# Kernel tuning notes

Hardware: AMD Instinct MI355X
Metric: run time of the kernel (lower is better)

The kernel has to match this reference:

```python
import jax, jax.numpy as jnp
import numpy as np

B, N, D, R, W, H, I = 256, 2048, 128, 4, 1, 1024, 1024
CI = I + R * D                       # controller input size (1536)
IF = 2 * D * W + 2 * W + 1 + 4 * R + D * R   # interface size (787)
OPI = H + R * D                      # output_proj input (1536)


def _norm(v):
    # F.normalize(dim=-1): x / max(||x||, eps)
    return v / jnp.maximum(jnp.linalg.norm(v, axis=-1, keepdims=True), 1e-12)


def setup_inputs() -> dict:
    key = jax.random.key(0)
    ks = jax.random.split(key, 16)
    u = lambda k, shape, fan: jax.random.uniform(k, shape, jnp.float32, -1.0 / np.sqrt(fan), 1.0 / np.sqrt(fan))
    return {
        "x": jax.random.normal(ks[0], (B, I), jnp.float32),
        "memory": jax.random.normal(ks[1], (N, D), jnp.float32) * np.sqrt(2.0 / (N + D)),  # xavier-ish
        "usage": jax.random.uniform(ks[2], (N,), jnp.float32),          # usage in [0,1)
        "link": jax.random.normal(ks[3], (N, N), jnp.float32) * 0.01,   # non-trivial link state
        "W_ih": u(ks[4], (4 * H, CI), H),
        "W_hh": u(ks[5], (4 * H, H), H),
        "b_ih": u(ks[6], (4 * H,), H),
        "b_hh": u(ks[7], (4 * H,), H),
        "W_if": u(ks[8], (IF, H), H),
        "b_if": u(ks[9], (IF,), H),
        "W_out": u(ks[10], (H, OPI), OPI),
        "b_out": u(ks[11], (H,), OPI),
    }


def reference(x, memory, usage, link, W_ih, W_hh, b_ih, b_hh, W_if, b_if, W_out, b_out):
    # initial uniform read weights (prev state at first step)
    prev_rw = jnp.full((B, R, N), 1.0 / N, x.dtype)
    read_flat = (prev_rw @ memory).reshape(B, -1)                 # (B, R*D)
    cin = jnp.concatenate([x, read_flat], axis=-1)                # (B, CI)

    # single LSTM step, h0 = c0 = 0, torch gate order i,f,g,o
    g = cin @ W_ih.T + b_ih + b_hh
    gi, gf, gg, go = jnp.split(g, 4, axis=-1)
    c = jax.nn.sigmoid(gi) * jnp.tanh(gg)
    h = jax.nn.sigmoid(go) * jnp.tanh(c)                          # (B, H) controller out

    itf = h @ W_if.T + b_if                                       # (B, IF)
    o = 0
    write_vals = itf[:, o:o + D * W].reshape(B, W, D); o += D * W
    erase = jax.nn.sigmoid(itf[:, o:o + D * W]).reshape(B, W, D); o += D * W
    write_gates = jax.nn.sigmoid(itf[:, o:o + W]); o += W         # (B, W)
    alloc_gate = jax.nn.sigmoid(itf[:, o:o + 1]); o += 1          # (B, 1)
    o += W                                                        # free gates (parsed, unused)
    read_modes = jax.nn.softmax(itf[:, o:o + 3 * R].reshape(B, R, 3), -1); o += 3 * R
    read_str = jax.nn.softplus(itf[:, o:o + R]); o += R           # (B, R)
    read_keys = itf[:, o:o + D * R].reshape(B, R, D)

    # content addressing for the write (strength = 1)
    mem_n = _norm(memory)
    cw = jax.nn.softmax(_norm(write_vals.mean(1)) @ mem_n.T, -1)  # (B, N)

    # allocation weighting: sorted-usage cumprod (per source semantics)
    idx = jnp.argsort(usage)
    su = usage[idx]
    cp = jnp.cumprod(1.0 - su)
    alloc_s = jnp.concatenate([su[:1], su[1:] * cp[:-1]])
    alloc = jnp.zeros_like(usage).at[idx].set(alloc_s)[None, :] * alloc_gate  # (B, N)

    write_w = write_gates[:, :, None] * (0.5 * cw + 0.5 * alloc)[:, None, :]  # (B, W, N)

    # temporal link update: batch-mean of diag-masked outer product, decay 0.9
    lu = jnp.einsum('bwn,bwm->nm', write_w, write_w) / B
    lu = lu * (1.0 - jnp.eye(N, dtype=lu.dtype))
    link_new = link * 0.9 + lu * 0.1

    # memory write (erase then add, batch-mean)
    ev = erase * write_gates[:, :, None]
    av = write_vals * write_gates[:, :, None]
    erase_mat = jnp.einsum('bwn,bwd->nd', write_w, ev) / B
    add_mat = jnp.einsum('bwn,bwd->nd', write_w, av) / B
    mem_new = memory * (1.0 - erase_mat) + add_mat

    # read addressing on updated memory and updated link (all R heads vectorized)
    sim = jnp.einsum('brd,nd->brn', _norm(read_keys), _norm(mem_new))
    content_r = jax.nn.softmax(sim * read_str[:, :, None], -1)    # (B, R, N)
    backward_w = jnp.einsum('brn,nm->brm', prev_rw, link_new)     # mode 1: prev @ L
    forward_w = jnp.einsum('brn,mn->brm', prev_rw, link_new)      # mode 2: prev @ L^T
    new_rw = (read_modes[..., 0:1] * content_r
              + read_modes[..., 1:2] * backward_w
              + read_modes[..., 2:3] * forward_w)                 # (B, R, N)

    read_out = (new_rw @ mem_new).reshape(B, -1)                  # (B, R*D)
    out = jnp.concatenate([h, read_out], axis=-1) @ W_out.T + b_out
    return out
```

## Files before the change

kernel.cpp:

```cpp
#include <hip/hip_runtime.h>
#include <cmath>

#define DEVI __device__ __forceinline__

DEVI float sigm(float x){ return 1.f/(1.f+expf(-x)); }

typedef __attribute__((ext_vector_type(8))) _Float16 half8;
typedef __attribute__((ext_vector_type(4))) _Float16 half4;
typedef __attribute__((ext_vector_type(4))) float float4v;


__global__ void k_zero(float* __restrict__ p, int n){
  int i = blockIdx.x*256 + threadIdx.x;
  if (i < n) p[i] = 0.f;
}

__global__ __launch_bounds__(256) void k_stage1(
    const float* __restrict__ mem, float* __restrict__ cm, _Float16* __restrict__ mem_h)
{
  __shared__ float smem[4][132];
  const int blk = blockIdx.x, t = threadIdx.x;
  const int wv = t >> 6, lane = t & 63;
  int rbase = blk*16 + wv*4;
  float x0[4], x1[4], ss[4];
  #pragma unroll
  for (int u = 0; u < 4; u++){
    const float* a = mem + (size_t)(rbase+u)*128;
    x0[u] = a[lane]; x1[u] = a[lane+64];
  }
  #pragma unroll
  for (int u = 0; u < 4; u++) ss[u] = x0[u]*x0[u] + x1[u]*x1[u];
  #pragma unroll
  for (int o = 1; o < 64; o <<= 1){
    #pragma unroll
    for (int u = 0; u < 4; u++) ss[u] += __shfl_xor(ss[u], o);
  }
  float c0 = 0.f, c1 = 0.f;
  #pragma unroll
  for (int u = 0; u < 4; u++){
    float invn = 1.f / fmaxf(sqrtf(ss[u]), 1e-12f);
    mem_h[(size_t)(rbase+u)*128 + lane]      = (_Float16)(x0[u]*invn);
    mem_h[(size_t)(rbase+u)*128 + 64 + lane] = (_Float16)(x1[u]*invn);
    c0 += x0[u]; c1 += x1[u];
  }
  smem[wv][lane] = c0; smem[wv][64+lane] = c1;
  __syncthreads();
  if (t < 128) atomicAdd(&cm[t], smem[0][t]+smem[1][t]+smem[2][t]+smem[3][t]);
}

#define QA 264
#define QB 520
#define QB3 776

template<typename TB> struct BReg;
template<> struct BReg<_Float16>{
  half8 v;
  DEVI void load(const _Float16* p){ v = *(const half8*)p; }
  DEVI half8 get() const { return v; }
};
template<> struct BReg<float>{
  float4v a, b;
  DEVI void load(const float* p){ a = *(const float4v*)p; b = *(const float4v*)(p+4); }
  DEVI half8 get() const {
    half8 h;
    #pragma unroll
    for (int j = 0; j < 4; j++){ h[j] = (_Float16)a[j]; h[4+j] = (_Float16)b[j]; }
    return h;
  }
};

struct ARegX {
  float4v a, b; float sc;
  DEVI void load(const float* __restrict__ x, const float* __restrict__ cm, int row, int k){
    const float* p;
    if (k < 1024){ p = x + (size_t)row*1024 + k; sc = 1.f; }
    else         { p = cm + ((k - 1024) & 127); sc = (1.f/2048.f); }
    a = *(const float4v*)p; b = *(const float4v*)(p+4);
  }
  DEVI half8 get() const {
    half8 h;
    #pragma unroll
    for (int j = 0; j < 4; j++){ h[j] = (_Float16)(a[j]*sc); h[4+j] = (_Float16)(b[j]*sc); }
    return h;
  }
};

template<typename TB>
__global__ __launch_bounds__(256) void gemm_t(
    const _Float16* __restrict__ A, const TB* __restrict__ Bm, float* __restrict__ C,
    int M, int N, int K,
    const float* __restrict__ bias1, const float* __restrict__ bias2)
{
  __shared__ _Float16 Ah[2][8*QA];
  __shared__ _Float16 Bh[2][8*QB];
  const int tid = threadIdx.x;
  const int m0 = blockIdx.y*32, n0 = blockIdx.x*64;
  const int T = K >> 6;
  const int arow = tid >> 3, aq = tid & 7;
  const int brow = tid >> 3, bq = tid & 7;
  int nB0 = n0 + brow;      if (nB0 >= N) nB0 = N - 1;
  int nB1 = n0 + brow + 32; if (nB1 >= N) nB1 = N - 1;
  const _Float16* Aptr = A + (size_t)(m0 + arow)*K + aq*8;
  const TB* Bp0 = Bm + (size_t)nB0*K + bq*8;
  const TB* Bp1 = Bm + (size_t)nB1*K + bq*8;
  const int wA  = aq*QA + arow*8;
  const int wB0 = bq*QB + brow*8;
  const int wB1 = bq*QB + (brow+32)*8;
  const int wv_ = tid >> 6, lane = tid & 63;
  const int fq = lane >> 4, fr = lane & 15;
  const int m16 = (wv_ & 1)*16, nb = (wv_ >> 1)*32;

  half8 ra;
  BReg<TB> rb0, rb1;
  ra = *(const half8*)(Aptr);
  rb0.load(Bp0);
  rb1.load(Bp1);
  *(half8*)&Ah[0][wA]  = ra;
  *(half8*)&Bh[0][wB0] = rb0.get();
  *(half8*)&Bh[0][wB1] = rb1.get();
  __syncthreads();

  float4v acc0 = {0.f,0.f,0.f,0.f}, acc1 = {0.f,0.f,0.f,0.f};
  for (int t = 0; t < T; t++){
    const int cur = t & 1, nxt = cur ^ 1;
    if (t+1 < T){
      ra = *(const half8*)(Aptr + (t+1)*64);
      rb0.load(Bp0 + (t+1)*64);
      rb1.load(Bp1 + (t+1)*64);
    }
    #pragma unroll
    for (int s = 0; s < 2; s++){
      int q = s*4 + fq;
      half8 a  = *(half8*)&Ah[cur][q*QA + (m16+fr)*8];
      half8 b0 = *(half8*)&Bh[cur][q*QB + (nb+fr)*8];
      half8 b1 = *(half8*)&Bh[cur][q*QB + (nb+16+fr)*8];
      acc0 = __builtin_amdgcn_mfma_f32_16x16x32_f16(a, b0, acc0, 0, 0, 0);
      acc1 = __builtin_amdgcn_mfma_f32_16x16x32_f16(a, b1, acc1, 0, 0, 0);
    }
    if (t+1 < T){
      *(half8*)&Ah[nxt][wA]  = ra;
      *(half8*)&Bh[nxt][wB0] = rb0.get();
      *(half8*)&Bh[nxt][wB1] = rb1.get();
    }
    __syncthreads();
  }

  const int colA = n0 + nb + fr, colB = colA + 16;
  #pragma unroll
  for (int i = 0; i < 4; i++){
    int m = m0 + m16 + fq*4 + i;
    if (colA < N){
      float v = acc0[i];
      if (bias1) v += bias1[colA];
      if (bias2) v += bias2[colA];
      C[(size_t)m*N + colA] = v;
    }
    if (colB < N){
      float v = acc1[i];
      if (bias1) v += bias1[colB];
      if (bias2) v += bias2[colB];
      C[(size_t)m*N + colB] = v;
    }
  }
}

__global__ __launch_bounds__(256) void gemm_hro(
    const _Float16* __restrict__ Ah_, const _Float16* __restrict__ Aro,
    const float* __restrict__ Bm, float* __restrict__ C,
    const float* __restrict__ bias1)
{
  __shared__ _Float16 Ah[2][8*QA];
  __shared__ _Float16 Bh[2][8*QB];
  const int tid = threadIdx.x;
  const int m0 = blockIdx.y*32, n0 = blockIdx.x*64;
  const int T = 24;
  const int arow = tid >> 3, aq = tid & 7;
  const int brow = tid >> 3, bq = tid & 7;
  const int arw = m0 + arow;
  const float* Bp0 = Bm + (size_t)(n0 + brow)*1536 + bq*8;
  const float* Bp1 = Bm + (size_t)(n0 + brow + 32)*1536 + bq*8;
  const int wA  = aq*QA + arow*8;
  const int wB0 = bq*QB + brow*8;
  const int wB1 = bq*QB + (brow+32)*8;
  const int wv_ = tid >> 6, lane = tid & 63;
  const int fq = lane >> 4, fr = lane & 15;
  const int m16 = (wv_ & 1)*16, nb = (wv_ >> 1)*32;

  auto ldA = [&](int k) -> half8 {
    const _Float16* p = (k < 1024) ? (Ah_ + (size_t)arw*1024 + k)
                                   : (Aro + (size_t)arw*512 + (k - 1024));
    return *(const half8*)p;
  };

  half8 ra;
  BReg<float> rb0, rb1;
  ra = ldA(aq*8);
  rb0.load(Bp0);
  rb1.load(Bp1);
  *(half8*)&Ah[0][wA]  = ra;
  *(half8*)&Bh[0][wB0] = rb0.get();
  *(half8*)&Bh[0][wB1] = rb1.get();
  __syncthreads();

  float4v acc0 = {0.f,0.f,0.f,0.f}, acc1 = {0.f,0.f,0.f,0.f};
  for (int t = 0; t < T; t++){
    const int cur = t & 1, nxt = cur ^ 1;
    if (t+1 < T){
      ra = ldA(aq*8 + (t+1)*64);
      rb0.load(Bp0 + (t+1)*64);
      rb1.load(Bp1 + (t+1)*64);
    }
    #pragma unroll
    for (int s = 0; s < 2; s++){
      int q = s*4 + fq;
      half8 a  = *(half8*)&Ah[cur][q*QA + (m16+fr)*8];
      half8 b0 = *(half8*)&Bh[cur][q*QB + (nb+fr)*8];
      half8 b1 = *(half8*)&Bh[cur][q*QB + (nb+16+fr)*8];
      acc0 = __builtin_amdgcn_mfma_f32_16x16x32_f16(a, b0, acc0, 0, 0, 0);
      acc1 = __builtin_amdgcn_mfma_f32_16x16x32_f16(a, b1, acc1, 0, 0, 0);
    }
    if (t+1 < T){
      *(half8*)&Ah[nxt][wA]  = ra;
      *(half8*)&Bh[nxt][wB0] = rb0.get();
      *(half8*)&Bh[nxt][wB1] = rb1.get();
    }
    __syncthreads();
  }

  const int colA = n0 + nb + fr, colB = colA + 16;
  #pragma unroll
  for (int i = 0; i < 4; i++){
    int m = m0 + m16 + fq*4 + i;
    C[(size_t)m*1024 + colA] = acc0[i] + bias1[colA];
    C[(size_t)m*1024 + colB] = acc1[i] + bias1[colB];
  }
}

__global__ __launch_bounds__(256) void k_gemm_wwExp(
    const _Float16* __restrict__ A, const _Float16* __restrict__ Bm,
    float* __restrict__ C, float* __restrict__ rsum)
{
  __shared__ _Float16 Ah[2][8*QA];
  __shared__ _Float16 Bh[2][8*QB];
  const int tid = threadIdx.x;
  const int m0 = blockIdx.y*32, n0 = blockIdx.x*64;
  const int arow = tid >> 3, aq = tid & 7;
  const int brow = tid >> 3, bq = tid & 7;
  const _Float16* Aptr = A + (size_t)(m0 + arow)*128 + aq*8;
  const _Float16* Bp0 = Bm + (size_t)(n0 + brow)*128 + bq*8;
  const _Float16* Bp1 = Bm + (size_t)(n0 + brow + 32)*128 + bq*8;
  const int wA  = aq*QA + arow*8;
  const int wB0 = bq*QB + brow*8;
  const int wB1 = bq*QB + (brow+32)*8;
  const int wv_ = tid >> 6, lane = tid & 63;
  const int fq = lane >> 4, fr = lane & 15;
  const int m16 = (wv_ & 1)*16, nb = (wv_ >> 1)*32;

  half8 ra  = *(const half8*)(Aptr);
  half8 rb0 = *(const half8*)(Bp0);
  half8 rb1 = *(const half8*)(Bp1);
  *(half8*)&Ah[0][wA]  = ra;
  *(half8*)&Bh[0][wB0] = rb0;
  *(half8*)&Bh[0][wB1] = rb1;
  __syncthreads();

  float4v acc0 = {0.f,0.f,0.f,0.f}, acc1 = {0.f,0.f,0.f,0.f};
  for (int t = 0; t < 2; t++){
    const int cur = t & 1, nxt = cur ^ 1;
    if (t == 0){
      ra  = *(const half8*)(Aptr + 64);
      rb0 = *(const half8*)(Bp0 + 64);
      rb1 = *(const half8*)(Bp1 + 64);
    }
    #pragma unroll
    for (int s = 0; s < 2; s++){
      int q = s*4 + fq;
      half8 a  = *(half8*)&Ah[cur][q*QA + (m16+fr)*8];
      half8 b0 = *(half8*)&Bh[cur][q*QB + (nb+fr)*8];
      half8 b1 = *(half8*)&Bh[cur][q*QB + (nb+16+fr)*8];
      acc0 = __builtin_amdgcn_mfma_f32_16x16x32_f16(a, b0, acc0, 0, 0, 0);
      acc1 = __builtin_amdgcn_mfma_f32_16x16x32_f16(a, b1, acc1, 0, 0, 0);
    }
    if (t == 0){
      *(half8*)&Ah[nxt][wA]  = ra;
      *(half8*)&Bh[nxt][wB0] = rb0;
      *(half8*)&Bh[nxt][wB1] = rb1;
    }
    __syncthreads();
  }

  const int colA = n0 + nb + fr, colB = colA + 16;
  #pragma unroll
  for (int i = 0; i < 4; i++){
    int m = m0 + m16 + fq*4 + i;
    float e0 = expf(acc0[i]);
    float e1 = expf(acc1[i]);
    C[(size_t)m*2048 + colA] = e0;
    C[(size_t)m*2048 + colB] = e1;
    float rs = e0 + e1;
    #pragma unroll
    for (int o = 1; o < 16; o <<= 1) rs += __shfl_xor(rs, o);
    if (fr == 0) atomicAdd(&rsum[m], rs);
  }
}

__global__ __launch_bounds__(256) void k_big2(
    const float* __restrict__ x, const float* __restrict__ cm,
    const float* __restrict__ W,
    const float* __restrict__ b_ih, const float* __restrict__ b_hh,
    _Float16* __restrict__ h,
    const float* __restrict__ usage, float* __restrict__ alloc,
    const float* __restrict__ link, float* __restrict__ rsl, float* __restrict__ cslp)
{
  extern __shared__ char smraw[];
  const int blk = blockIdx.x, tid = threadIdx.x;
  const int wv = tid >> 6, lane = tid & 63;

  if (blk < 256){
    _Float16* AhP = (_Float16*)smraw;
    _Float16* BhP = (_Float16*)(smraw + 2*8*QA*sizeof(_Float16));
    const int SA = 8*QA, SB = 8*QB3;
    const int m0 = (blk >> 5)*32, c0 = (blk & 31)*32;
    const int T = 24;
    const int arow = tid >> 3, aq = tid & 7;
    const int brow = tid >> 3, bq = tid & 7;
    const int arw = m0 + arow;
    const float* Bpi = W + (size_t)(       c0 + brow)*1536 + bq*8;
    const float* Bpg = W + (size_t)(2048 + c0 + brow)*1536 + bq*8;
    const float* Bpo = W + (size_t)(3072 + c0 + brow)*1536 + bq*8;
    const int wA  = aq*QA + arow*8;
    const int wBi = bq*QB3 + brow*8;
    const int wBg = bq*QB3 + (32+brow)*8;
    const int wBo = bq*QB3 + (64+brow)*8;
    const int fq = lane >> 4, fr = lane & 15;
    const int m16 = (wv & 1)*16, c16 = (wv >> 1)*16;

    ARegX ax0, ax1;
    BReg<float> ri0, rg0, ro0, ri1, rg1, ro1;
    ax0.load(x, cm, arw, aq*8);
    ri0.load(Bpi); rg0.load(Bpg); ro0.load(Bpo);
    ax1.load(x, cm, arw, aq*8 + 64);
    ri1.load(Bpi + 64); rg1.load(Bpg + 64); ro1.load(Bpo + 64);
    *(half8*)&AhP[wA]  = ax0.get();
    *(half8*)&BhP[wBi] = ri0.get();
    *(half8*)&BhP[wBg] = rg0.get();
    *(half8*)&BhP[wBo] = ro0.get();
    __syncthreads();

    float4v acci = {0.f,0.f,0.f,0.f}, accg = {0.f,0.f,0.f,0.f}, acco = {0.f,0.f,0.f,0.f};
    for (int t = 0; t < T; t++){
      const int cur = t & 1, nxt = cur ^ 1;
      if (t+2 < T){
        if (cur == 0){
          ax0.load(x, cm, arw, aq*8 + (t+2)*64);
          ri0.load(Bpi + (t+2)*64); rg0.load(Bpg + (t+2)*64); ro0.load(Bpo + (t+2)*64);
        } else {
          ax1.load(x, cm, arw, aq*8 + (t+2)*64);
          ri1.load(Bpi + (t+2)*64); rg1.load(Bpg + (t+2)*64); ro1.load(Bpo + (t+2)*64);
        }
      }
      #pragma unroll
      for (int s = 0; s < 2; s++){
        int q = s*4 + fq;
        half8 a  = *(half8*)&AhP[cur*SA + q*QA + (m16+fr)*8];
        half8 bi = *(half8*)&BhP[cur*SB + q*QB3 + (c16+fr)*8];
        half8 bg = *(half8*)&BhP[cur*SB + q*QB3 + (32+c16+fr)*8];
        half8 bo = *(half8*)&BhP[cur*SB + q*QB3 + (64+c16+fr)*8];
        acci = __builtin_amdgcn_mfma_f32_16x16x32_f16(a, bi, acci, 0, 0, 0);
        accg = __builtin_amdgcn_mfma_f32_16x16x32_f16(a, bg, accg, 0, 0, 0);
        acco = __builtin_amdgcn_mfma_f32_16x16x32_f16(a, bo, acco, 0, 0, 0);
      }
      if (t+1 < T){
        if (nxt == 1){
          *(half8*)&AhP[SA + wA]  = ax1.get();
          *(half8*)&BhP[SB + wBi] = ri1.get();
          *(half8*)&BhP[SB + wBg] = rg1.get();
          *(half8*)&BhP[SB + wBo] = ro1.get();
        } else {
          *(half8*)&AhP[wA]  = ax0.get();
          *(half8*)&BhP[wBi] = ri0.get();
          *(half8*)&BhP[wBg] = rg0.get();
          *(half8*)&BhP[wBo] = ro0.get();
        }
      }
      __syncthreads();
    }

    const int col = c0 + c16 + fr;
    const float bi1 = b_ih[col]        + b_hh[col];
    const float bg1 = b_ih[2048 + col] + b_hh[2048 + col];
    const float bo1 = b_ih[3072 + col] + b_hh[3072 + col];
    #pragma unroll
    for (int i = 0; i < 4; i++){
      int m = m0 + m16 + fq*4 + i;
      float gi = acci[i] + bi1;
      float gg = accg[i] + bg1;
      float go = acco[i] + bo1;
      float c = sigm(gi) * tanhf(gg);
      h[(size_t)m*1024 + col] = (_Float16)(sigm(go) * tanhf(c));
    }
  } else if (blk < 512){
    float (*smem)[132] = (float(*)[132])smraw;
    int pb = blk - 256;
    int r0 = pb*8;
    int c0 = tid*8;
    float4v v0[8], v1[8];
    #pragma unroll
    for (int u = 0; u < 8; u++){
      const float* lp = link + (size_t)(r0+u)*2048 + c0;
      v0[u] = *(const float4v*)lp;
      v1[u] = *(const float4v*)(lp+4);
    }
    float colacc[8];
    #pragma unroll
    for (int j = 0; j < 8; j++) colacc[j] = 0.f;
    float rowpart[8];
    #pragma unroll
    for (int u = 0; u < 8; u++){
      float s = 0.f;
      #pragma unroll
      for (int j = 0; j < 4; j++){
        colacc[j]   += v0[u][j]; colacc[4+j] += v1[u][j];
        s += v0[u][j] + v1[u][j];
      }
      rowpart[u] = s;
    }
    #pragma unroll
    for (int o = 1; o < 64; o <<= 1){
      #pragma unroll
      for (int u = 0; u < 8; u++) rowpart[u] += __shfl_xor(rowpart[u], o);
    }
    if (lane == 0){
      #pragma unroll
      for (int u = 0; u < 8; u++) smem[wv][u] = rowpart[u];
    }
    __syncthreads();
    if (tid < 8) rsl[r0+tid] = smem[0][tid]+smem[1][tid]+smem[2][tid]+smem[3][tid];
    float4v w0, w1;
    #pragma unroll
    for (int j = 0; j < 4; j++){ w0[j] = colacc[j]; w1[j] = colacc[4+j]; }
    *(float4v*)&cslp[(size_t)pb*2048 + c0]     = w0;
    *(float4v*)&cslp[(size_t)pb*2048 + c0 + 4] = w1;
  } else {
    int n = (blk - 512)*4 + wv;
    float un = usage[n];
    float prod = 1.f;
    #pragma unroll
    for (int i = 0; i < 32; i++){
      int m = lane + i*64;
      float um = usage[m];
      bool before = (um < un) || (um == un && m < n);
      prod *= before ? (1.f - um) : 1.f;
    }
    #pragma unroll
    for (int o = 32; o > 0; o >>= 1) prod *= __shfl_xor(prod, o);
    if (lane == 0) alloc[n] = un * prod;
  }
}

DEVI float blockReduce128(float v, float* lds2){
  #pragma unroll
  for (int o = 32; o > 0; o >>= 1) v += __shfl_xor(v, o);
  int w = threadIdx.x >> 6;
  __syncthreads();
  if ((threadIdx.x & 63) == 0) lds2[w] = v;
  __syncthreads();
  return lds2[0] + lds2[1];
}

__global__ __launch_bounds__(128) void k_parse(const float* __restrict__ itf,
    _Float16* __restrict__ wv_h, float* __restrict__ ev, float* __restrict__ av,
    float* __restrict__ wg_, float* __restrict__ ag_,
    float* __restrict__ rm0, float* __restrict__ rm1, float* __restrict__ rm2,
    _Float16* __restrict__ rks_h)
{
  __shared__ float red[2];
  int b = blockIdx.x, t = threadIdx.x;
  const float* it = itf + (size_t)b*787;
  float wg = sigm(it[256]);
  float ag = sigm(it[257]);
  if (t == 0){ wg_[b] = wg; ag_[b] = ag; }
  float w = it[t];
  av[b*128 + t] = w * wg;
  ev[b*128 + t] = sigm(it[128 + t]) * wg;
  float ss = blockReduce128(w*w, red);
  float invwv = 1.f / fmaxf(sqrtf(ss), 1e-12f);
  wv_h[b*128 + t] = (_Float16)(w * invwv);
  if (t < 4){
    int rr = t;
    float m0v = it[259 + rr*3 + 0], m1v = it[259 + rr*3 + 1], m2v = it[259 + rr*3 + 2];
    float mx = fmaxf(m0v, fmaxf(m1v, m2v));
    float e0 = expf(m0v - mx), e1 = expf(m1v - mx), e2 = expf(m2v - mx);
    float inv = 1.f / (e0 + e1 + e2);
    rm0[b*4 + rr] = e0*inv; rm1[b*4 + rr] = e1*inv; rm2[b*4 + rr] = e2*inv;
  }
  #pragma unroll
  for (int rr = 0; rr < 4; rr++){
    float kv = it[275 + rr*128 + t];
    float ks = blockReduce128(kv*kv, red);
    float sx = it[271 + rr];
    float str = fmaxf(sx, 0.f) + log1pf(expf(-fabsf(sx)));
    float invk = 1.f / fmaxf(sqrtf(ks), 1e-12f);
    rks_h[((size_t)b*4 + rr)*128 + t] = (_Float16)(kv * invk * str);
  }
}

__global__ __launch_bounds__(256) void k_memupdate_fused(const float* __restrict__ ww,
    const float* __restrict__ ev, const float* __restrict__ av,
    const float* __restrict__ mem,
    const float* __restrict__ wg, const float* __restrict__ ag,
    const float* __restrict__ alloc, const float* __restrict__ rsum,
    const float* __restrict__ rsl, const float* __restrict__ cslp,
    _Float16* __restrict__ memn_h, _Float16* __restrict__ memnT_h,
    float* __restrict__ bwm, float* __restrict__ fwm)
{
  __shared__ float Ws[16][34];
  __shared__ float Es[16][132], Vs[16][132];
  __shared__ float lb[128], lf[128];
  __shared__ _Float16 Traw[32][132];
  __shared__ float tbs[256], c1s[256], c2s[256];
  __shared__ float allocL[32];
  __shared__ float sq[8][32], sd[8][32];
  __shared__ float cpart[8][32];
  __shared__ float bwL[32], fwL[32];
  __shared__ float sred[4];
  const int n0 = blockIdx.x*32;
  const int tid = threadIdx.x, tx = tid & 31, ty = tid >> 5;

  {
    float sa = 0.f;
    #pragma unroll
    for (int i = 0; i < 8; i++) sa += alloc[tid + i*256];
    #pragma unroll
    for (int o = 32; o > 0; o >>= 1) sa += __shfl_xor(sa, o);
    if ((tid & 63) == 0) sred[tid >> 6] = sa;
    if (tid < 128){ lb[tid] = 0.f; lf[tid] = 0.f; }
    if (tid < 32) allocL[tid] = alloc[n0 + tid];
    __syncthreads();
    sa = (sred[0]+sred[1]) + (sred[2]+sred[3]);
    float w = wg[tid], a = ag[tid];
    tbs[tid] = w*(0.5f + 0.5f*a*sa);
    c1s[tid] = 0.5f*w / rsum[tid];
    c2s[tid] = 0.5f*w*a;
  }
  {
    int col = n0 + tx;
    float s = 0.f;
    for (int p = ty*32; p < ty*32 + 32; p += 4){
      s += cslp[(size_t)(p+0)*2048 + col] + cslp[(size_t)(p+1)*2048 + col]
         + cslp[(size_t)(p+2)*2048 + col] + cslp[(size_t)(p+3)*2048 + col];
    }
    cpart[ty][tx] = s;
  }
  __syncthreads();

  const int wk = tid >> 4, wn = (tid & 15)*2;
  const int ek = tid >> 4, ec = (tid & 15)*8;
  float ae[4][4] = {}, aa[4][4] = {};
  float qp = 0.f, ddp = 0.f;
  for (int k0 = 0; k0 < 256; k0 += 16){
    float2 vw  = *(const float2*)(ww + (size_t)(k0+wk)*2048 + n0 + wn);
    float4 ve0 = *(const float4*)(ev + (size_t)(k0+ek)*128 + ec);
    float4 ve1 = *(const float4*)(ev + (size_t)(k0+ek)*128 + ec + 4);
    float4 va0 = *(const float4*)(av + (size_t)(k0+ek)*128 + ec);
    float4 va1 = *(const float4*)(av + (size_t)(k0+ek)*128 + ec + 4);
    __syncthreads();
    {
      float cb1 = c1s[k0+wk], cb2 = c2s[k0+wk];
      Ws[wk][wn]   = cb1*vw.x + cb2*allocL[wn];
      Ws[wk][wn+1] = cb1*vw.y + cb2*allocL[wn+1];
    }
    *(float4*)&Es[ek][ec] = ve0; *(float4*)&Es[ek][ec+4] = ve1;
    *(float4*)&Vs[ek][ec] = va0; *(float4*)&Vs[ek][ec+4] = va1;
    __syncthreads();
    #pragma unroll
    for (int k = 0; k < 16; k++){
      float a[4], e[4], v[4];
      #pragma unroll
      for (int i = 0; i < 4; i++) a[i] = Ws[k][ty*4+i];
      #pragma unroll
      for (int j = 0; j < 4; j++){ e[j] = Es[k][tx*4+j]; v[j] = Vs[k][tx*4+j]; }
      #pragma unroll
      for (int i = 0; i < 4; i++)
        #pragma unroll
        for (int j = 0; j < 4; j++){
          ae[i][j] = fmaf(a[i], e[j], ae[i][j]);
          aa[i][j] = fmaf(a[i], v[j], aa[i][j]);
        }
    }
    {
      float w0 = Ws[ty*2+0][tx], w1 = Ws[ty*2+1][tx];
      qp  = fmaf(tbs[k0+ty*2+0], w0, qp);  ddp = fmaf(w0, w0, ddp);
      qp  = fmaf(tbs[k0+ty*2+1], w1, qp);  ddp = fmaf(w1, w1, ddp);
    }
  }
  sq[ty][tx] = qp; sd[ty][tx] = ddp;
  __syncthreads();
  if (tid < 32){
    float q = 0.f, dd = 0.f, cs = 0.f;
    #pragma unroll
    for (int z = 0; z < 8; z++){ q += sq[z][tid]; dd += sd[z][tid]; cs += cpart[z][tid]; }
    float lus = (q - dd) * (1.f/256.f);
    bwL[tid] = (0.9f*cs + 0.1f*lus) * (1.f/2048.f);
    fwL[tid] = (0.9f*rsl[n0+tid] + 0.1f*lus) * (1.f/2048.f);
  }
  __syncthreads();

  float ab[4] = {0,0,0,0}, af[4] = {0,0,0,0};
  #pragma unroll
  for (int i = 0; i < 4; i++){
    int n = n0 + ty*4 + i;
    float bwn = bwL[ty*4+i], fwn = fwL[ty*4+i];
    float v[4]; float ss = 0.f;
    #pragma unroll
    for (int j = 0; j < 4; j++){
      int d = tx*4 + j;
      float em = ae[i][j]*(1.f/256.f), am = aa[i][j]*(1.f/256.f);
      float mv = mem[(size_t)n*128 + d]*(1.f - em) + am;
      v[j] = mv; ss += mv*mv;
      ab[j] = fmaf(bwn, mv, ab[j]);
      af[j] = fmaf(fwn, mv, af[j]);
    }
    #pragma unroll
    for (int o = 1; o < 32; o <<= 1) ss += __shfl_xor(ss, o);
    float invn = 1.f / fmaxf(sqrtf(ss), 1e-12f);
    half4 hn, hr;
    #pragma unroll
    for (int j = 0; j < 4; j++){ hn[j] = (_Float16)(v[j]*invn); hr[j] = (_Float16)v[j]; }
    *(half4*)(memn_h + (size_t)n*128 + tx*4) = hn;
    *(half4*)&Traw[ty*4+i][tx*4] = hr;
  }
  __syncthreads();
  {
    int d = tid >> 1, seg = (tid & 1)*16;
    half8 o0, o1;
    #pragma unroll
    for (int j = 0; j < 8; j++){ o0[j] = Traw[seg+j][d]; o1[j] = Traw[seg+8+j][d]; }
    *(half8*)(memnT_h + (size_t)d*2048 + n0 + seg)     = o0;
    *(half8*)(memnT_h + (size_t)d*2048 + n0 + seg + 8) = o1;
  }
  #pragma unroll
  for (int j = 0; j < 4; j++){
    atomicAdd(&lb[tx*4+j], ab[j]);
    atomicAdd(&lf[tx*4+j], af[j]);
  }
  __syncthreads();
  if (tid < 128){
    atomicAdd(&bwm[tid], lb[tid]);
    atomicAdd(&fwm[tid], lf[tid]);
  }
}

__global__ __launch_bounds__(256) void k_flash(
    const _Float16* __restrict__ Q, const _Float16* __restrict__ Kh,
    const _Float16* __restrict__ Vt,
    float* __restrict__ pacc, float* __restrict__ pm, float* __restrict__ pl)
{
  __shared__ _Float16 Pl[4][16][32];
  __shared__ float cmb[4][2080];
  __shared__ float scl[4][16];
  const int tid = threadIdx.x;
  const int qt = blockIdx.x >> 2, kc = blockIdx.x & 3;
  const int wv = tid >> 6, lane = tid & 63;
  const int fq = lane >> 4, fr = lane & 15;
  const int kw0 = kc*512 + wv*128;

  half8 aq[4];
  #pragma unroll
  for (int c = 0; c < 4; c++)
    aq[c] = *(const half8*)(Q + (size_t)(qt*16 + fr)*128 + c*32 + fq*8);

  float m[4] = {-3.0e38f,-3.0e38f,-3.0e38f,-3.0e38f};
  float l[4] = {0.f,0.f,0.f,0.f};
  float4v acc[8] = {};
  for (int s = 0; s < 4; s++){
    const int kb = kw0 + s*32;
    float4v S0 = {0,0,0,0}, S1 = {0,0,0,0};
    #pragma unroll
    for (int c = 0; c < 4; c++){
      half8 b0 = *(const half8*)(Kh + (size_t)(kb + fr)*128      + c*32 + fq*8);
      half8 b1 = *(const half8*)(Kh + (size_t)(kb + 16 + fr)*128 + c*32 + fq*8);
      S0 = __builtin_amdgcn_mfma_f32_16x16x32_f16(aq[c], b0, S0, 0, 0, 0);
      S1 = __builtin_amdgcn_mfma_f32_16x16x32_f16(aq[c], b1, S1, 0, 0, 0);
    }
    float mt[4], ps[4];
    #pragma unroll
    for (int i = 0; i < 4; i++) mt[i] = fmaxf(S0[i], S1[i]);
    #pragma unroll
    for (int o = 1; o < 16; o <<= 1){
      #pragma unroll
      for (int i = 0; i < 4; i++) mt[i] = fmaxf(mt[i], __shfl_xor(mt[i], o));
    }
    #pragma unroll
    for (int i = 0; i < 4; i++){
      float mn = fmaxf(m[i], mt[i]);
      float al = expf(m[i] - mn);
      float p0 = expf(S0[i] - mn), p1 = expf(S1[i] - mn);
      S0[i] = p0; S1[i] = p1;
      ps[i] = p0 + p1;
      l[i] *= al;
      m[i] = mn;
      #pragma unroll
      for (int c = 0; c < 8; c++) acc[c][i] *= al;
    }
    #pragma unroll
    for (int o = 1; o < 16; o <<= 1){
      #pragma unroll
      for (int i = 0; i < 4; i++) ps[i] += __shfl_xor(ps[i], o);
    }
    #pragma unroll
    for (int i = 0; i < 4; i++) l[i] += ps[i];
    #pragma unroll
    for (int i = 0; i < 4; i++){
      Pl[wv][fq*4+i][fr]      = (_Float16)S0[i];
      Pl[wv][fq*4+i][16 + fr] = (_Float16)S1[i];
    }
    half8 pf = *(half8*)&Pl[wv][fr][fq*8];
    #pragma unroll
    for (int c = 0; c < 8; c++){
      half8 bv = *(const half8*)(Vt + (size_t)(c*16 + fr)*2048 + kb + fq*8);
      acc[c] = __builtin_amdgcn_mfma_f32_16x16x32_f16(pf, bv, acc[c], 0, 0, 0);
    }
  }
  if (fr == 0){
    #pragma unroll
    for (int i = 0; i < 4; i++){
      cmb[wv][fq*4+i]      = m[i];
      cmb[wv][16 + fq*4+i] = l[i];
    }
  }
  #pragma unroll
  for (int c = 0; c < 8; c++)
    #pragma unroll
    for (int i = 0; i < 4; i++)
      cmb[wv][32 + (fq*4+i)*128 + c*16 + fr] = acc[c][i];
  __syncthreads();
  if (tid < 16){
    float mm = fmaxf(fmaxf(cmb[0][tid], cmb[1][tid]), fmaxf(cmb[2][tid], cmb[3][tid]));
    float ll = 0.f;
    #pragma unroll
    for (int w = 0; w < 4; w++){
      float e = expf(cmb[w][tid] - mm);
      scl[w][tid] = e;
      ll += e * cmb[w][16 + tid];
    }
    pm[blockIdx.x*16 + tid] = mm;
    pl[blockIdx.x*16 + tid] = ll;
  }
  __syncthreads();
  for (int e = tid; e < 2048; e += 256){
    int q = e >> 7;
    float a = scl[0][q]*cmb[0][32+e] + scl[1][q]*cmb[1][32+e]
            + scl[2][q]*cmb[2][32+e] + scl[3][q]*cmb[3][32+e];
    pacc[(size_t)blockIdx.x*2048 + e] = a;
  }
}

__global__ void k_ro(const float* __restrict__ pacc, const float* __restrict__ pm,
                     const float* __restrict__ pl,
                     const float* __restrict__ rm0, const float* __restrict__ rm1,
                     const float* __restrict__ rm2, const float* __restrict__ bwm,
                     const float* __restrict__ fwm, _Float16* __restrict__ ro){
  int idx = blockIdx.x*256 + threadIdx.x;
  int row = idx >> 7, d = idx & 127;
  int qt = row >> 4, q = row & 15;
  float mm = -3.0e38f;
  #pragma unroll
  for (int kc = 0; kc < 4; kc++) mm = fmaxf(mm, pm[(qt*4+kc)*16 + q]);
  float num = 0.f, den = 0.f;
  #pragma unroll
  for (int kc = 0; kc < 4; kc++){
    float e = expf(pm[(qt*4+kc)*16 + q] - mm);
    den += e * pl[(qt*4+kc)*16 + q];
    num += e * pacc[(size_t)(qt*4+kc)*2048 + q*128 + d];
  }
  float pv = num / den;
  ro[idx] = (_Float16)(rm0[row]*pv + rm1[row]*bwm[d] + rm2[row]*fwm[d]);
}


extern "C" void kernel_launch(void* const* d_in, const int* in_sizes, int n_in,
                              void* d_out, int out_size, void* d_ws, size_t ws_size,
                              hipStream_t stream)
{
  const float* x     = (const float*)d_in[0];
  const float* mem   = (const float*)d_in[1];
  const float* usage = (const float*)d_in[2];
  const float* link  = (const float*)d_in[3];
  const float* W_ih  = (const float*)d_in[4];
  const float* b_ih  = (const float*)d_in[6];
  const float* b_hh  = (const float*)d_in[7];
  const float* W_if  = (const float*)d_in[8];
  const float* b_if  = (const float*)d_in[9];
  const float* W_out = (const float*)d_in[10];
  const float* b_out = (const float*)d_in[11];
  float* out = (float*)d_out;
  float* ws  = (float*)d_ws;

  float* cm     = ws + 0;
  float* bwm    = ws + 2176;
  float* fwm    = ws + 2304;
  float* rsum   = ws + 2432;
  float* wg     = ws + 6784;
  float* ag     = ws + 7040;
  float* rm0    = ws + 7296;
  float* rm1    = ws + 8320;
  float* rm2    = ws + 9344;
  float* alloc  = ws + 10368;
  float* rsl    = ws + 12416;
  float* ev     = ws + 14464;
  float* av     = ws + 47232;
  float* itf    = ws + 1128576;
  float* ww     = ws + 1330048;
  float* pacc   = ws + 1854336;
  float* pm     = ws + 2378624;
  float* pl     = ws + 2382720;
  _Float16* wv_h    = (_Float16*)(ws + 2386816);
  _Float16* mem_h   = (_Float16*)(ws + 2403200);
  _Float16* memn_h  = (_Float16*)(ws + 2534272);
  _Float16* memnT_h = (_Float16*)(ws + 2665344);
  _Float16* rks_h   = (_Float16*)(ws + 2796416);
  _Float16* ro_h    = (_Float16*)(ws + 2861952);
  _Float16* h_h     = (_Float16*)(ws + 3255168);
  float* cslp       = ws + 3386240;

  const int SH_BIG2 = (2*8*QA + 2*8*QB3) * (int)sizeof(_Float16);

  k_zero<<<11, 256, 0, stream>>>(ws, 2688);

  k_stage1<<<128, 256, 0, stream>>>(mem, cm, mem_h);

  k_big2<<<1024, 256, SH_BIG2, stream>>>(x, cm, W_ih, b_ih, b_hh, h_h,
                                         usage, alloc, link, rsl, cslp);

  gemm_t<float><<<dim3(13,8), 256, 0, stream>>>(h_h, W_if, itf, 256, 787, 1024, b_if, nullptr);
  k_parse<<<256, 128, 0, stream>>>(itf, wv_h, ev, av, wg, ag, rm0, rm1, rm2, rks_h);

  k_gemm_wwExp<<<dim3(32,8), 256, 0, stream>>>(wv_h, mem_h, ww, rsum);

  k_memupdate_fused<<<64, 256, 0, stream>>>(ww, ev, av, mem, wg, ag, alloc, rsum,
                                            rsl, cslp, memn_h, memnT_h, bwm, fwm);

  k_flash<<<256, 256, 0, stream>>>(rks_h, memn_h, memnT_h, pacc, pm, pl);

  k_ro<<<512, 256, 0, stream>>>(pacc, pm, pl, rm0, rm1, rm2, bwm, fwm, ro_h);
  gemm_hro<<<dim3(16,8), 256, 0, stream>>>(h_h, ro_h, W_out, out, b_out);

  (void)in_sizes; (void)n_in; (void)out_size; (void)ws_size;
}
```

Baseline: 230.2 us.

## Deepen GEMM global prefetch to two stages and split flash over 8 key chunks

The two MFMA GEMM kernels now keep two sets of prefetch registers, so global loads are issued two k-tiles ahead instead of one, which hides more memory latency. The flash read kernel splits the 2048 memory rows into 8 chunks per query tile instead of 4, doubling its block count to fill more CUs. The reduction in k_ro and the workspace offsets are updated to match. In exchange the GEMMs use more registers and there is more partial-result traffic to combine.

```diff
diff --git a/kernel.cpp b/kernel.cpp
--- a/kernel.cpp
+++ b/kernel.cpp
@@ -110,23 +110,30 @@
   const int fq = lane >> 4, fr = lane & 15;
   const int m16 = (wv_ & 1)*16, nb = (wv_ >> 1)*32;
 
-  half8 ra;
-  BReg<TB> rb0, rb1;
-  ra = *(const half8*)(Aptr);
-  rb0.load(Bp0);
-  rb1.load(Bp1);
-  *(half8*)&Ah[0][wA]  = ra;
-  *(half8*)&Bh[0][wB0] = rb0.get();
-  *(half8*)&Bh[0][wB1] = rb1.get();
+  half8 ra0, ra1;
+  BReg<TB> rb00, rb10, rb01, rb11;
+  ra0 = *(const half8*)(Aptr);
+  rb00.load(Bp0); rb10.load(Bp1);
+  if (T > 1){
+    ra1 = *(const half8*)(Aptr + 64);
+    rb01.load(Bp0 + 64); rb11.load(Bp1 + 64);
+  }
+  *(half8*)&Ah[0][wA]  = ra0;
+  *(half8*)&Bh[0][wB0] = rb00.get();
+  *(half8*)&Bh[0][wB1] = rb10.get();
   __syncthreads();
 
   float4v acc0 = {0.f,0.f,0.f,0.f}, acc1 = {0.f,0.f,0.f,0.f};
   for (int t = 0; t < T; t++){
     const int cur = t & 1, nxt = cur ^ 1;
-    if (t+1 < T){
-      ra = *(const half8*)(Aptr + (t+1)*64);
-      rb0.load(Bp0 + (t+1)*64);
-      rb1.load(Bp1 + (t+1)*64);
+    if (t+2 < T){
+      if (cur == 0){
+        ra0 = *(const half8*)(Aptr + (t+2)*64);
+        rb00.load(Bp0 + (t+2)*64); rb10.load(Bp1 + (t+2)*64);
+      } else {
+        ra1 = *(const half8*)(Aptr + (t+2)*64);
+        rb01.load(Bp0 + (t+2)*64); rb11.load(Bp1 + (t+2)*64);
+      }
     }
     #pragma unroll
     for (int s = 0; s < 2; s++){
@@ -138,9 +145,15 @@
       acc1 = __builtin_amdgcn_mfma_f32_16x16x32_f16(a, b1, acc1, 0, 0, 0);
     }
     if (t+1 < T){
-      *(half8*)&Ah[nxt][wA]  = ra;
-      *(half8*)&Bh[nxt][wB0] = rb0.get();
-      *(half8*)&Bh[nxt][wB1] = rb1.get();
+      if (nxt == 1){
+        *(half8*)&Ah[1][wA]  = ra1;
+        *(half8*)&Bh[1][wB0] = rb01.get();
+        *(half8*)&Bh[1][wB1] = rb11.get();
+      } else {
+        *(half8*)&Ah[0][wA]  = ra0;
+        *(half8*)&Bh[0][wB0] = rb00.get();
+        *(half8*)&Bh[0][wB1] = rb10.get();
+      }
     }
     __syncthreads();
   }
@@ -192,23 +205,28 @@
     return *(const half8*)p;
   };
 
-  half8 ra;
-  BReg<float> rb0, rb1;
-  ra = ldA(aq*8);
-  rb0.load(Bp0);
-  rb1.load(Bp1);
-  *(half8*)&Ah[0][wA]  = ra;
-  *(half8*)&Bh[0][wB0] = rb0.get();
-  *(half8*)&Bh[0][wB1] = rb1.get();
+  half8 ra0, ra1;
+  BReg<float> rb00, rb10, rb01, rb11;
+  ra0 = ldA(aq*8);
+  rb00.load(Bp0); rb10.load(Bp1);
+  ra1 = ldA(aq*8 + 64);
+  rb01.load(Bp0 + 64); rb11.load(Bp1 + 64);
+  *(half8*)&Ah[0][wA]  = ra0;
+  *(half8*)&Bh[0][wB0] = rb00.get();
+  *(half8*)&Bh[0][wB1] = rb10.get();
   __syncthreads();
 
   float4v acc0 = {0.f,0.f,0.f,0.f}, acc1 = {0.f,0.f,0.f,0.f};
   for (int t = 0; t < T; t++){
     const int cur = t & 1, nxt = cur ^ 1;
-    if (t+1 < T){
-      ra = ldA(aq*8 + (t+1)*64);
-      rb0.load(Bp0 + (t+1)*64);
-      rb1.load(Bp1 + (t+1)*64);
+    if (t+2 < T){
+      if (cur == 0){
+        ra0 = ldA(aq*8 + (t+2)*64);
+        rb00.load(Bp0 + (t+2)*64); rb10.load(Bp1 + (t+2)*64);
+      } else {
+        ra1 = ldA(aq*8 + (t+2)*64);
+        rb01.load(Bp0 + (t+2)*64); rb11.load(Bp1 + (t+2)*64);
+      }
     }
     #pragma unroll
     for (int s = 0; s < 2; s++){
@@ -220,9 +238,15 @@
       acc1 = __builtin_amdgcn_mfma_f32_16x16x32_f16(a, b1, acc1, 0, 0, 0);
     }
     if (t+1 < T){
-      *(half8*)&Ah[nxt][wA]  = ra;
-      *(half8*)&Bh[nxt][wB0] = rb0.get();
-      *(half8*)&Bh[nxt][wB1] = rb1.get();
+      if (nxt == 1){
+        *(half8*)&Ah[1][wA]  = ra1;
+        *(half8*)&Bh[1][wB0] = rb01.get();
+        *(half8*)&Bh[1][wB1] = rb11.get();
+      } else {
+        *(half8*)&Ah[0][wA]  = ra0;
+        *(half8*)&Bh[0][wB0] = rb00.get();
+        *(half8*)&Bh[0][wB1] = rb10.get();
+      }
     }
     __syncthreads();
   }
@@ -660,10 +684,10 @@
   __shared__ float cmb[4][2080];
   __shared__ float scl[4][16];
   const int tid = threadIdx.x;
-  const int qt = blockIdx.x >> 2, kc = blockIdx.x & 3;
+  const int qt = blockIdx.x >> 3, kc = blockIdx.x & 7;
   const int wv = tid >> 6, lane = tid & 63;
   const int fq = lane >> 4, fr = lane & 15;
-  const int kw0 = kc*512 + wv*128;
+  const int kw0 = kc*256 + wv*64;
 
   half8 aq[4];
   #pragma unroll
@@ -673,7 +697,7 @@
   float m[4] = {-3.0e38f,-3.0e38f,-3.0e38f,-3.0e38f};
   float l[4] = {0.f,0.f,0.f,0.f};
   float4v acc[8] = {};
-  for (int s = 0; s < 4; s++){
+  for (int s = 0; s < 2; s++){
     const int kb = kw0 + s*32;
     float4v S0 = {0,0,0,0}, S1 = {0,0,0,0};
     #pragma unroll
@@ -766,13 +790,13 @@
   int qt = row >> 4, q = row & 15;
   float mm = -3.0e38f;
   #pragma unroll
-  for (int kc = 0; kc < 4; kc++) mm = fmaxf(mm, pm[(qt*4+kc)*16 + q]);
+  for (int kc = 0; kc < 8; kc++) mm = fmaxf(mm, pm[(qt*8+kc)*16 + q]);
   float num = 0.f, den = 0.f;
   #pragma unroll
-  for (int kc = 0; kc < 4; kc++){
-    float e = expf(pm[(qt*4+kc)*16 + q] - mm);
-    den += e * pl[(qt*4+kc)*16 + q];
-    num += e * pacc[(size_t)(qt*4+kc)*2048 + q*128 + d];
+  for (int kc = 0; kc < 8; kc++){
+    float e = expf(pm[(qt*8+kc)*16 + q] - mm);
+    den += e * pl[(qt*8+kc)*16 + q];
+    num += e * pacc[(size_t)(qt*8+kc)*2048 + q*128 + d];
   }
   float pv = num / den;
   ro[idx] = (_Float16)(rm0[row]*pv + rm1[row]*bwm[d] + rm2[row]*fwm[d]);
@@ -813,16 +837,16 @@
   float* itf    = ws + 1128576;
   float* ww     = ws + 1330048;
   float* pacc   = ws + 1854336;
-  float* pm     = ws + 2378624;
-  float* pl     = ws + 2382720;
-  _Float16* wv_h    = (_Float16*)(ws + 2386816);
-  _Float16* mem_h   = (_Float16*)(ws + 2403200);
-  _Float16* memn_h  = (_Float16*)(ws + 2534272);
-  _Float16* memnT_h = (_Float16*)(ws + 2665344);
-  _Float16* rks_h   = (_Float16*)(ws + 2796416);
-  _Float16* ro_h    = (_Float16*)(ws + 2861952);
-  _Float16* h_h     = (_Float16*)(ws + 3255168);
-  float* cslp       = ws + 3386240;
+  float* pm     = ws + 2902912;
+  float* pl     = ws + 2911104;
+  _Float16* wv_h    = (_Float16*)(ws + 2919296);
+  _Float16* mem_h   = (_Float16*)(ws + 2935680);
+  _Float16* memn_h  = (_Float16*)(ws + 3066752);
+  _Float16* memnT_h = (_Float16*)(ws + 3197824);
+  _Float16* rks_h   = (_Float16*)(ws + 3328896);
+  _Float16* ro_h    = (_Float16*)(ws + 3394432);
+  _Float16* h_h     = (_Float16*)(ws + 3459968);
+  float* cslp       = ws + 3591040;
 
   const int SH_BIG2 = (2*8*QA + 2*8*QB3) * (int)sizeof(_Float16);
 
@@ -841,7 +865,7 @@
   k_memupdate_fused<<<64, 256, 0, stream>>>(ww, ev, av, mem, wg, ag, alloc, rsum,
                                             rsl, cslp, memn_h, memnT_h, bwm, fwm);
 
-  k_flash<<<256, 256, 0, stream>>>(rks_h, memn_h, memnT_h, pacc, pm, pl);
+  k_flash<<<512, 256, 0, stream>>>(rks_h, memn_h, memnT_h, pacc, pm, pl);
 
   k_ro<<<512, 256, 0, stream>>>(pacc, pm, pl, rm0, rm1, rm2, bwm, fwm, ro_h);
   gemm_hro<<<dim3(16,8), 256, 0, stream>>>(h_h, ro_h, W_out, out, b_out);
```

Result: no change. 230.1 us (-0.0%).
